# Optimization experiments

Hardware: AMD Instinct MI355X
Metric: run time of the kernel (lower is better)

The kernel has to match this reference:

```python
import jax, jax.numpy as jnp
import numpy as np

B, N, HID, H = 2, 2048, 2048, 16
DH = HID // H  # 128


def _rope_tables(n, d, base=10000.0):
    inv_freq = 1.0 / (base ** (np.arange(0, d, 2, dtype=np.float32) / d))
    t = np.arange(n, dtype=np.float32)
    freqs = np.outer(t, inv_freq)                 # [N, d/2]
    emb = np.concatenate([freqs, freqs], axis=-1)  # [N, d]
    return jnp.asarray(np.cos(emb)), jnp.asarray(np.sin(emb))


def setup_inputs() -> dict:
    key = jax.random.key(0)
    k1, k2, k3 = jax.random.split(key, 3)
    std = 1.0 / HID ** 0.5
    cos, sin = _rope_tables(N, DH)
    return {
        "hidden_states": jax.random.normal(k1, (B, N, HID), dtype=jnp.float32),
        "cos": cos,
        "sin": sin,
        "w_qkv": (jax.random.truncated_normal(k2, -2.0, 2.0, (3 * HID, HID), jnp.float32) * std),
        "w_o": (jax.random.truncated_normal(k3, -2.0, 2.0, (HID, HID), jnp.float32) * std),
    }


def _rotate_half(x):
    d = x.shape[-1] // 2
    return jnp.concatenate([-x[..., d:], x[..., :d]], axis=-1)


def reference(hidden_states, cos, sin, w_qkv, w_o):
    b, n, _ = hidden_states.shape
    qkv = (hidden_states @ w_qkv.T).reshape(b, n, 3, H, DH)
    q, k, v = qkv[:, :, 0], qkv[:, :, 1], qkv[:, :, 2]  # [B,N,H,DH]
    c = cos[:, None, :]  # [N,1,DH] broadcasts over heads
    s = sin[:, None, :]
    q = q * c + _rotate_half(q) * s
    k = k * c + _rotate_half(k) * s
    scale = 1.0 / jnp.sqrt(jnp.asarray(DH, q.dtype))
    scores = jnp.einsum("bqhd,bkhd->bhqk", q, k) * scale
    attn = jax.nn.softmax(scores, axis=-1)
    out = jnp.einsum("bhqk,bkhd->bqhd", attn, v).reshape(b, n, HID)
    return out @ w_o.T
```

## Files before the change

kernel.cpp:

```cpp
#include <hip/hip_runtime.h>
#include <math.h>

#define NB 2
#define NN 2048
#define HIDDEN 2048
#define NHEAD 16
#define DHEAD 128

typedef __attribute__((ext_vector_type(8))) short bf16x8;
typedef __attribute__((ext_vector_type(4))) float floatx4;

static __device__ __forceinline__ short f2bf(float f) {
    union { float f; unsigned u; } v; v.f = f;
    unsigned r = v.u + 0x7fffu + ((v.u >> 16) & 1u);
    return (short)(r >> 16);
}
static __device__ __forceinline__ void gload_lds16(const short* g, short* l) {
    __builtin_amdgcn_global_load_lds(
        (const __attribute__((address_space(1))) void*)g,
        (__attribute__((address_space(3))) void*)l, 16, 0, 0);
}

__global__ __launch_bounds__(256) void cast_bf16_3(
    const float* __restrict__ a, const float* __restrict__ b, const float* __restrict__ c,
    short* __restrict__ oa, short* __restrict__ ob, short* __restrict__ oc,
    int n4a, int n4b, int n4c)
{
    int i = blockIdx.x * 256 + threadIdx.x;
    const float* s; short* d; int j;
    if (i < n4a) { s = a; d = oa; j = i; }
    else if (i < n4a + n4b) { s = b; d = ob; j = i - n4a; }
    else if (i < n4a + n4b + n4c) { s = c; d = oc; j = i - n4a - n4b; }
    else return;
    float4 v = ((const float4*)s)[j];
    short4 o;
    o.x = f2bf(v.x); o.y = f2bf(v.y); o.z = f2bf(v.z); o.w = f2bf(v.w);
    ((short4*)d)[j] = o;
}

template <int MODE>
__global__ __launch_bounds__(256) void gemm_bf16_nt(
    const short* __restrict__ A, const short* __restrict__ Bw,
    const float* __restrict__ cosT, const float* __restrict__ sinT,
    short* __restrict__ Qp, short* __restrict__ Kp, short* __restrict__ Vtp,
    float* __restrict__ Cp, int M, int N, int K)
{
    __shared__ short As[128 * 32];
    __shared__ short Bs[128 * 32];

    const int tid = threadIdx.x;
    const int w = tid >> 6;
    const int l = tid & 63;
    const int quad = l >> 4;
    const int l15 = l & 15;
    const int bm = blockIdx.y * 128;
    const int bn = blockIdx.x * 128;

    const int srow = l >> 2;
    const int schunk = (l & 3) * 8;

    const int wm = (w & 1) * 64;
    const int wn2 = w >> 1;

    floatx4 acc[4][4];
#pragma unroll
    for (int i = 0; i < 4; ++i)
#pragma unroll
        for (int j = 0; j < 4; ++j) acc[i][j] = (floatx4){0.f, 0.f, 0.f, 0.f};

    for (int k0 = 0; k0 < K; k0 += 32) {
        __syncthreads();
#pragma unroll
        for (int r = 0; r < 2; ++r) {
            int row = r * 64 + w * 16 + srow;
            gload_lds16(A + (size_t)(bm + row) * K + k0 + schunk, &As[row * 32 + schunk]);
            gload_lds16(Bw + (size_t)(bn + row) * K + k0 + schunk, &Bs[row * 32 + schunk]);
        }
        __syncthreads();

        bf16x8 af[4], bf[4];
#pragma unroll
        for (int i = 0; i < 4; ++i)
            af[i] = *(const bf16x8*)&As[(wm + i * 16 + l15) * 32 + quad * 8];
#pragma unroll
        for (int j = 0; j < 4; ++j) {
            int col = wn2 * 32 + (j & 1) * 16 + ((j >> 1) << 6);
            bf[j] = *(const bf16x8*)&Bs[(col + l15) * 32 + quad * 8];
        }
#pragma unroll
        for (int i = 0; i < 4; ++i)
#pragma unroll
            for (int j = 0; j < 4; ++j)
                acc[i][j] = __builtin_amdgcn_mfma_f32_16x16x32_bf16(af[i], bf[j], acc[i][j], 0, 0, 0);
    }

    if (MODE == 1) {
#pragma unroll
        for (int i = 0; i < 4; ++i) {
#pragma unroll
            for (int reg = 0; reg < 4; ++reg) {
                int row = bm + wm + i * 16 + quad * 4 + reg;
                float* crow = Cp + (size_t)row * N + bn;
#pragma unroll
                for (int j = 0; j < 4; ++j)
                    crow[wn2 * 32 + (j & 1) * 16 + ((j >> 1) << 6) + l15] = acc[i][j][reg];
            }
        }
    } else {
        const int which = bn >> 11;
        const int head = (bn >> 7) & (NHEAD - 1);
        const float qsc = (which == 0) ? 0.12751791525f : 1.0f;
#pragma unroll
        for (int i = 0; i < 4; ++i) {
#pragma unroll
            for (int reg = 0; reg < 4; ++reg) {
                int m = bm + wm + i * 16 + quad * 4 + reg;
                int b = m >> 11, n = m & (NN - 1);
                int bh = b * NHEAD + head;
                if (which == 2) {
#pragma unroll
                    for (int j = 0; j < 4; ++j) {
                        int d = wn2 * 32 + (j & 1) * 16 + ((j >> 1) << 6) + l15;
                        Vtp[((size_t)bh * DHEAD + d) * NN + n] = f2bf(acc[i][j][reg]);
                    }
                } else {
                    short* dst = (which == 0 ? Qp : Kp) + ((size_t)bh * NN + n) * DHEAD;
#pragma unroll
                    for (int j = 0; j < 2; ++j) {
                        int d0 = wn2 * 32 + j * 16 + l15;
                        float c = cosT[(size_t)n * DHEAD + d0];
                        float s = sinT[(size_t)n * DHEAD + d0];
                        float e0 = acc[i][j][reg], e1 = acc[i][j + 2][reg];
                        dst[d0]      = f2bf((e0 * c - e1 * s) * qsc);
                        dst[d0 + 64] = f2bf((e1 * c + e0 * s) * qsc);
                    }
                }
            }
        }
    }
}

__global__ __launch_bounds__(256, 2) void attn_mfma(
    const short* __restrict__ Qb, const short* __restrict__ Kb,
    const short* __restrict__ Vt, short* __restrict__ AOb)
{
    __shared__ __align__(16) short Ks[64 * 128];
    __shared__ __align__(16) short Vs[128 * 64];
    __shared__ __align__(16) short Ps[4][32][72];

    const int tid = threadIdx.x;
    const int w = tid >> 6;
    const int l = tid & 63;
    const int quad = l >> 4;
    const int l15 = l & 15;
    const int bh = blockIdx.y;
    const int qt = blockIdx.x * 128;

    const short* Qg = Qb + (size_t)bh * NN * DHEAD;
    const short* Kg = Kb + (size_t)bh * NN * DHEAD;
    const short* Vg = Vt + (size_t)bh * DHEAD * NN;

    bf16x8 qf[2][4];
#pragma unroll
    for (int mi = 0; mi < 2; ++mi) {
        const short* qrow = Qg + (size_t)(qt + w * 32 + mi * 16 + l15) * DHEAD + quad * 8;
#pragma unroll
        for (int kc = 0; kc < 4; ++kc) qf[mi][kc] = *(const bf16x8*)(qrow + kc * 32);
    }

    floatx4 of[2][8];
#pragma unroll
    for (int mi = 0; mi < 2; ++mi)
#pragma unroll
        for (int dc = 0; dc < 8; ++dc) of[mi][dc] = (floatx4){0.f, 0.f, 0.f, 0.f};
    float ls[2][4] = {{0.f, 0.f, 0.f, 0.f}, {0.f, 0.f, 0.f, 0.f}};

    for (int kt = 0; kt < NN; kt += 64) {
        __syncthreads();

#pragma unroll
        for (int rr = 0; rr < 4; ++rr) {
            int s = (w * 4 + rr) * 64 + l;
            int row = s >> 4;
            int j = (s & 15) ^ (row & 15);
            gload_lds16(Kg + (size_t)(kt + row) * DHEAD + j * 8, &Ks[s * 8]);
        }
#pragma unroll
        for (int rr = 0; rr < 4; ++rr) {
            int s = (w * 4 + rr) * 64 + l;
            int row = s >> 3;
            int c = (s & 7) ^ (row & 7);
            gload_lds16(Vg + (size_t)row * NN + kt + c * 8, &Vs[s * 8]);
        }
        __syncthreads();

#pragma unroll
        for (int mi = 0; mi < 2; ++mi) {
            floatx4 sf[4];
#pragma unroll
            for (int n16 = 0; n16 < 4; ++n16) {
                floatx4 acc = (floatx4){0.f, 0.f, 0.f, 0.f};
                const short* kbase = &Ks[(n16 * 16 + l15) * 128];
#pragma unroll
                for (int kc = 0; kc < 4; ++kc)
                    acc = __builtin_amdgcn_mfma_f32_16x16x32_bf16(
                              qf[mi][kc], *(const bf16x8*)&kbase[((4 * kc + quad) ^ l15) * 8],
                              acc, 0, 0, 0);
                sf[n16] = acc;
            }
#pragma unroll
            for (int n16 = 0; n16 < 4; ++n16)
#pragma unroll
                for (int r = 0; r < 4; ++r) {
                    float p = exp2f(sf[n16][r]);
                    ls[mi][r] += p;
                    Ps[w][mi * 16 + quad * 4 + r][n16 * 16 + l15] = f2bf(p);
                }
            bf16x8 pa[2];
#pragma unroll
            for (int kc = 0; kc < 2; ++kc)
                pa[kc] = *(const bf16x8*)&Ps[w][mi * 16 + l15][kc * 32 + quad * 8];
#pragma unroll
            for (int dc = 0; dc < 8; ++dc) {
                int row = dc * 16 + l15;
#pragma unroll
                for (int kc = 0; kc < 2; ++kc) {
                    int c = (kc * 4 + quad) ^ (row & 7);
                    of[mi][dc] = __builtin_amdgcn_mfma_f32_16x16x32_bf16(
                                     pa[kc], *(const bf16x8*)&Vs[row * 64 + c * 8],
                                     of[mi][dc], 0, 0, 0);
                }
            }
        }
    }

    const int b = bh >> 4, h = bh & (NHEAD - 1);
#pragma unroll
    for (int mi = 0; mi < 2; ++mi)
#pragma unroll
        for (int r = 0; r < 4; ++r) {
            float s = ls[mi][r];
            s += __shfl_xor(s, 1, 64);
            s += __shfl_xor(s, 2, 64);
            s += __shfl_xor(s, 4, 64);
            s += __shfl_xor(s, 8, 64);
            float inv = 1.0f / s;
            int row = qt + w * 32 + mi * 16 + quad * 4 + r;
            short* dst = AOb + ((size_t)(b * NN + row)) * HIDDEN + h * DHEAD;
#pragma unroll
            for (int dc = 0; dc < 8; ++dc)
                dst[dc * 16 + l15] = f2bf(of[mi][dc][r] * inv);
        }
}

extern "C" void kernel_launch(void* const* d_in, const int* in_sizes, int n_in,
                              void* d_out, int out_size, void* d_ws, size_t ws_size,
                              hipStream_t stream)
{
    const float* hs = (const float*)d_in[0];
    const float* cosT = (const float*)d_in[1];
    const float* sinT = (const float*)d_in[2];
    const float* wqkv = (const float*)d_in[3];
    const float* wo = (const float*)d_in[4];
    float* out = (float*)d_out;

    const size_t N_HS = (size_t)NB * NN * HIDDEN;
    const size_t N_WQ = (size_t)3 * HIDDEN * HIDDEN;
    const size_t N_WO = (size_t)HIDDEN * HIDDEN;
    const size_t SZ = (size_t)NB * NHEAD * NN * DHEAD;

    short* Ahs   = (short*)d_ws;
    short* Wqkvb = Ahs + N_HS;
    short* Wob   = Wqkvb + N_WQ;
    short* Qb    = Wob + N_WO;
    short* Kb    = Qb + SZ;
    short* Vtb   = Kb + SZ;
    short* AOb   = Vtb + SZ;

    {
        int n4a = (int)(N_HS / 4), n4b = (int)(N_WQ / 4), n4c = (int)(N_WO / 4);
        int total = n4a + n4b + n4c;
        cast_bf16_3<<<(total + 255) / 256, 256, 0, stream>>>(
            hs, wqkv, wo, Ahs, Wqkvb, Wob, n4a, n4b, n4c);
    }
    {
        dim3 grid(3 * HIDDEN / 128, NB * NN / 128);
        gemm_bf16_nt<0><<<grid, 256, 0, stream>>>(
            Ahs, Wqkvb, cosT, sinT, Qb, Kb, Vtb, nullptr,
            NB * NN, 3 * HIDDEN, HIDDEN);
    }
    {
        dim3 grid(NN / 128, NB * NHEAD);
        attn_mfma<<<grid, 256, 0, stream>>>(Qb, Kb, Vtb, AOb);
    }
    {
        dim3 grid(HIDDEN / 128, NB * NN / 128);
        gemm_bf16_nt<1><<<grid, 256, 0, stream>>>(
            AOb, Wob, nullptr, nullptr, nullptr, nullptr, nullptr, out,
            NB * NN, HIDDEN, HIDDEN);
    }
}
```

Measured before the change: 474.5 us.

## Pad GEMM LDS rows and reuse K/V fragments across query sub-tiles

The GEMM stages A and B tiles into one shared buffer whose rows are padded to five 16-byte chunks. This is meant to avoid LDS bank conflicts on the MFMA fragment reads, and the global-to-LDS addresses are precomputed once outside the k-loop. The attention inner loop is reordered so each K and V fragment is read from LDS once and used for both query sub-tiles, which halves the LDS reads for K and V. The cost is higher register pressure from holding both sub-tiles' scores and P fragments at the same time, plus a few redundant padding loads.

```diff
diff --git a/kernel.cpp b/kernel.cpp
--- a/kernel.cpp
+++ b/kernel.cpp
@@ -45,8 +45,7 @@
     short* __restrict__ Qp, short* __restrict__ Kp, short* __restrict__ Vtp,
     float* __restrict__ Cp, int M, int N, int K)
 {
-    __shared__ short As[128 * 32];
-    __shared__ short Bs[128 * 32];
+    __shared__ __align__(16) short AB[1280 * 8];
 
     const int tid = threadIdx.x;
     const int w = tid >> 6;
@@ -56,12 +55,23 @@
     const int bm = blockIdx.y * 128;
     const int bn = blockIdx.x * 128;
 
-    const int srow = l >> 2;
-    const int schunk = (l & 3) * 8;
-
     const int wm = (w & 1) * 64;
     const int wn2 = w >> 1;
 
+    const short* gptr[5];
+    short* lptr[5];
+#pragma unroll
+    for (int r5 = 0; r5 < 5; ++r5) {
+        int s = r5 * 256 + tid;
+        int m = (s < 640) ? s : s - 640;
+        int row = m / 5;
+        int ch = m - row * 5;
+        if (ch == 4) ch = 0;
+        gptr[r5] = ((s < 640) ? (A + (size_t)(bm + row) * K)
+                              : (Bw + (size_t)(bn + row) * K)) + ch * 8;
+        lptr[r5] = &AB[s * 8];
+    }
+
     floatx4 acc[4][4];
 #pragma unroll
     for (int i = 0; i < 4; ++i)
@@ -71,21 +81,18 @@
     for (int k0 = 0; k0 < K; k0 += 32) {
         __syncthreads();
 #pragma unroll
-        for (int r = 0; r < 2; ++r) {
-            int row = r * 64 + w * 16 + srow;
-            gload_lds16(A + (size_t)(bm + row) * K + k0 + schunk, &As[row * 32 + schunk]);
-            gload_lds16(Bw + (size_t)(bn + row) * K + k0 + schunk, &Bs[row * 32 + schunk]);
-        }
+        for (int r5 = 0; r5 < 5; ++r5)
+            gload_lds16(gptr[r5] + k0, lptr[r5]);
         __syncthreads();
 
         bf16x8 af[4], bf[4];
 #pragma unroll
         for (int i = 0; i < 4; ++i)
-            af[i] = *(const bf16x8*)&As[(wm + i * 16 + l15) * 32 + quad * 8];
+            af[i] = *(const bf16x8*)&AB[((wm + i * 16 + l15) * 5 + quad) * 8];
 #pragma unroll
         for (int j = 0; j < 4; ++j) {
             int col = wn2 * 32 + (j & 1) * 16 + ((j >> 1) << 6);
-            bf[j] = *(const bf16x8*)&Bs[(col + l15) * 32 + quad * 8];
+            bf[j] = *(const bf16x8*)&AB[(640 + (col + l15) * 5 + quad) * 8];
         }
 #pragma unroll
         for (int i = 0; i < 4; ++i)
@@ -177,7 +184,6 @@
 
     for (int kt = 0; kt < NN; kt += 64) {
         __syncthreads();
-
 #pragma unroll
         for (int rr = 0; rr < 4; ++rr) {
             int s = (w * 4 + rr) * 64 + l;
@@ -194,42 +200,52 @@
         }
         __syncthreads();
 
-#pragma unroll
-        for (int mi = 0; mi < 2; ++mi) {
-            floatx4 sf[4];
-#pragma unroll
-            for (int n16 = 0; n16 < 4; ++n16) {
+        floatx4 sf[2][4];
+#pragma unroll
+        for (int n16 = 0; n16 < 4; ++n16) {
+            bf16x8 kf[4];
+            const short* kbase = &Ks[(n16 * 16 + l15) * 128];
+#pragma unroll
+            for (int kc = 0; kc < 4; ++kc)
+                kf[kc] = *(const bf16x8*)&kbase[((4 * kc + quad) ^ l15) * 8];
+#pragma unroll
+            for (int mi = 0; mi < 2; ++mi) {
                 floatx4 acc = (floatx4){0.f, 0.f, 0.f, 0.f};
-                const short* kbase = &Ks[(n16 * 16 + l15) * 128];
 #pragma unroll
                 for (int kc = 0; kc < 4; ++kc)
-                    acc = __builtin_amdgcn_mfma_f32_16x16x32_bf16(
-                              qf[mi][kc], *(const bf16x8*)&kbase[((4 * kc + quad) ^ l15) * 8],
-                              acc, 0, 0, 0);
-                sf[n16] = acc;
+                    acc = __builtin_amdgcn_mfma_f32_16x16x32_bf16(qf[mi][kc], kf[kc], acc, 0, 0, 0);
+                sf[mi][n16] = acc;
             }
+        }
+
+#pragma unroll
+        for (int mi = 0; mi < 2; ++mi)
 #pragma unroll
             for (int n16 = 0; n16 < 4; ++n16)
 #pragma unroll
                 for (int r = 0; r < 4; ++r) {
-                    float p = exp2f(sf[n16][r]);
+                    float p = exp2f(sf[mi][n16][r]);
                     ls[mi][r] += p;
                     Ps[w][mi * 16 + quad * 4 + r][n16 * 16 + l15] = f2bf(p);
                 }
-            bf16x8 pa[2];
+
+        bf16x8 pa[2][2];
+#pragma unroll
+        for (int mi = 0; mi < 2; ++mi)
 #pragma unroll
             for (int kc = 0; kc < 2; ++kc)
-                pa[kc] = *(const bf16x8*)&Ps[w][mi * 16 + l15][kc * 32 + quad * 8];
-#pragma unroll
-            for (int dc = 0; dc < 8; ++dc) {
-                int row = dc * 16 + l15;
-#pragma unroll
-                for (int kc = 0; kc < 2; ++kc) {
-                    int c = (kc * 4 + quad) ^ (row & 7);
+                pa[mi][kc] = *(const bf16x8*)&Ps[w][mi * 16 + l15][kc * 32 + quad * 8];
+
+#pragma unroll
+        for (int dc = 0; dc < 8; ++dc) {
+            int row = dc * 16 + l15;
+#pragma unroll
+            for (int kc = 0; kc < 2; ++kc) {
+                bf16x8 vf = *(const bf16x8*)&Vs[row * 64 + (((kc * 4 + quad) ^ (row & 7)) * 8)];
+#pragma unroll
+                for (int mi = 0; mi < 2; ++mi)
                     of[mi][dc] = __builtin_amdgcn_mfma_f32_16x16x32_bf16(
-                                     pa[kc], *(const bf16x8*)&Vs[row * 64 + c * 8],
-                                     of[mi][dc], 0, 0, 0);
-                }
+                                     pa[mi][kc], vf, of[mi][dc], 0, 0, 0);
             }
         }
     }
```

Result: faster. 463.7 us (-2.3%).
